# Kernel tuning notes

Measured on AMD Instinct MI355X. Metric: run time of the kernel, lower is better.

Reference implementation:

```python
import jax, jax.numpy as jnp
import numpy as np

STRIDE = (1, 2, 2)
PADDING = ((2, 2), (3, 3), (3, 3))


def setup_inputs() -> dict:
    key = jax.random.key(0)
    kx, kw, kb = jax.random.split(key, 3)
    x = jax.random.normal(kx, (8, 3, 16, 112, 112), dtype=jnp.float32)
    weight = jax.random.normal(kw, (64, 3, 5, 7, 7), dtype=jnp.float32)
    bias = jax.random.normal(kb, (64,), dtype=jnp.float32)
    return {"x": x, "weight": weight, "bias": bias}


def reference(x, weight, bias):
    # NCDHW input, OIDHW weight -> NCDHW output; same math as the
    # torch module's explicit slice-multiply-sum conv3d.
    out = jax.lax.conv_general_dilated(
        x, weight,
        window_strides=STRIDE,
        padding=PADDING,
        dimension_numbers=("NCDHW", "OIDHW", "NCDHW"),
    )
    out = out + bias[None, :, None, None, None]
    return out
```

## Files before the change

### kernel.cpp

```cpp
#include <hip/hip_runtime.h>


typedef __attribute__((ext_vector_type(8)))  short short8;
typedef __attribute__((ext_vector_type(4)))  float f32x4;
typedef __attribute__((ext_vector_type(16))) float f32x16;

#define CI 3
#define DI 16
#define HI 112
#define WI 112
#define CO 64
#define DO_ 16
#define HO 56
#define WO 56
#define HW_IN 12544
#define DHWO 50176

#define NROW 105
#define NCH 27

#define XP_ROW 120
#define XP_H   119
#define XP_D   20
#define XPAD_BYTES  (8*3*XP_D*XP_H*XP_ROW*2)
#define WBUF_OFF    XPAD_BYTES
#define WS_NEED     (WBUF_OFF + NCH*4*64*16 + 4096)

#define LR 13
#define SEG_SH (LR*XP_ROW)
#define SEG_DW (SEG_SH/2)
#define ROW_DW (XP_ROW/2)
#define ALDS_SH (18*SEG_SH + 128)

__device__ __forceinline__ unsigned short f2bf(float f) {
    unsigned u = __float_as_uint(f);
    return (unsigned short)((u + 0x7FFFu + ((u >> 16) & 1u)) >> 16);
}
__device__ __forceinline__ unsigned pk_bf16(float a, float b) {
    unsigned r;
    asm("v_cvt_pk_bf16_f32 %0, %1, %2" : "=v"(r) : "v"(a), "v"(b));
    return r;
}

__device__ __forceinline__ constexpr int rb2(int r) {
    const int rc = (r > 104) ? 104 : r;
    const int c  = rc / 35;
    const int kd = (rc / 7) % 5;
    const int kh = rc % 7;
    return (c * 6 + kd) * SEG_DW + kh * ROW_DW;
}

#define XP_THREADS (8*3*XP_D*XP_H*15)
#define XP_BLOCKS  3347

__global__ void prep_all(const float* __restrict__ x, const float* __restrict__ wgt,
                         unsigned* __restrict__ xp, short8* __restrict__ wbuf) {
    if (blockIdx.x < XP_BLOCKS) {
        const int g = blockIdx.x * 256 + threadIdx.x;
        if (g >= XP_THREADS) return;
        const int s8 = g % 15;
        int r = g / 15;
        const int hp = r % XP_H; r /= XP_H;
        const int dp = r % XP_D; r /= XP_D;
        const int c  = r % 3;
        const int n  = r / 3;
        const int din = dp - 2, hin = hp - 3;
        const bool rowok = ((unsigned)din < (unsigned)DI) && ((unsigned)hin < (unsigned)HI);
        float v[8];
        const int w0 = 8 * s8 - 3;
        if (rowok && s8 >= 1 && s8 <= 13) {
            const float* xr = x + ((n * CI + c) * DI + din) * HW_IN + hin * WI + w0;
            #pragma unroll
            for (int j = 0; j < 8; ++j) v[j] = xr[j];
        } else if (rowok && (s8 == 0 || s8 == 14)) {
            const float* xr = x + ((n * CI + c) * DI + din) * HW_IN + hin * WI;
            #pragma unroll
            for (int j = 0; j < 8; ++j) {
                const int w = w0 + j;
                v[j] = ((unsigned)w < (unsigned)WI) ? xr[w] : 0.0f;
            }
        } else {
            #pragma unroll
            for (int j = 0; j < 8; ++j) v[j] = 0.0f;
        }
        uint4 o;
        o.x = pk_bf16(v[0], v[1]); o.y = pk_bf16(v[2], v[3]);
        o.z = pk_bf16(v[4], v[5]); o.w = pk_bf16(v[6], v[7]);
        *reinterpret_cast<uint4*>(xp + 4 * (size_t)g) = o;
    } else {
        const int t = (blockIdx.x - XP_BLOCKS) * 256 + threadIdx.x;
        const int lane = t & 63;
        const int cf   = t >> 6;
        const int q    = cf & 3;
        const int a    = q & 1;
        const int ks   = q >> 1;
        const int ch   = cf >> 2;
        const int l31  = lane & 31;
        const int hl   = lane >> 5;
        const int co   = a * 32 + l31;
        const int r    = ch * 4 + ks * 2 + hl;
        const int rc   = (r > 104) ? 104 : r;
        const int c    = rc / 35;
        const int kd   = (rc / 7) % 5;
        const int kh   = rc % 7;
        const float* wsrc = wgt + (((co * CI + c) * 5 + kd) * 7 + kh) * 7;
        short8 v;
        #pragma unroll
        for (int j = 0; j < 8; ++j) {
            float w = (r < NROW && j < 7) ? wsrc[j] : 0.0f;
            v[j] = (short)f2bf(w);
        }
        wbuf[(size_t)cf * 64 + lane] = v;
    }
}

#define MFMA32(A, B, C) __builtin_amdgcn_mfma_f32_32x32x16_bf16(A, B, C, 0, 0, 0)
#define GLDS(src, dst) __builtin_amdgcn_global_load_lds( \
    (const __attribute__((address_space(1))) void*)(src), \
    (__attribute__((address_space(3))) void*)(dst), 16, 0, 0)

__launch_bounds__(512, 4)
__global__ void conv3d_v19(const unsigned short* __restrict__ xpad,
                           const short8* __restrict__ wbuf,
                           const float* __restrict__ bias,
                           float* __restrict__ out) {
    __shared__ __align__(16) unsigned short xl[ALDS_SH + 4 * 2048];

    const int tid = threadIdx.x;
    int b = ((blockIdx.x & 7) * 112) + (blockIdx.x >> 3);
    const int ht  = b % 14;  b /= 14;
    const int ddp = b & 7;
    const int n   = b >> 3;
    const int ho0 = ht * 4;
    const int dd0 = ddp * 2;

    const int lane = tid & 63;
    const int wid  = tid >> 6;

    {
        const size_t nb = (size_t)(n * CI) * XP_D;
        for (int s = wid; s < 18; s += 8) {
            const int c = s / 6;
            const int p = s - c * 6;
            const char* gsrc = (const char*)(xpad +
                ((nb + (size_t)c * XP_D + (dd0 + p)) * XP_H + 2 * ho0) * XP_ROW)
                + lane * 16;
            char* ldst = (char*)&xl[s * SEG_SH];
            GLDS(gsrc, ldst);
            GLDS(gsrc + 1024, ldst + 1024);
            GLDS(gsrc + 2048, ldst + 2048);
            if (lane < 3) GLDS(gsrc + 3072, ldst + 3072);
        }
    }
    if (wid == 0) {
        const char* gs = (const char*)wbuf + lane * 16;
        char* ad = (char*)&xl[ALDS_SH];
        GLDS(gs, ad); GLDS(gs + 1024, ad + 1024);
        GLDS(gs + 2048, ad + 2048); GLDS(gs + 3072, ad + 3072);
    } else if (wid == 1) {
        const char* gs = (const char*)(wbuf + 4 * 64) + lane * 16;
        char* ad = (char*)&xl[ALDS_SH] + 4096;
        GLDS(gs, ad); GLDS(gs + 1024, ad + 1024);
        GLDS(gs + 2048, ad + 2048); GLDS(gs + 3072, ad + 3072);
    }
    __syncthreads();

    const int ddl = wid & 1;
    const int hp  = wid >> 1;
    const int l31 = lane & 31;
    const int hl  = lane >> 5;
    const int tspB = ddl * SEG_DW + hp * (2 * ROW_DW) + l31;

    f32x16 acc[2][2];
    #pragma unroll
    for (int a = 0; a < 2; ++a) {
        f32x16 bv;
        #pragma unroll
        for (int g = 0; g < 16; ++g)
            bv[g] = bias[a * 32 + (g & 3) + 8 * (g >> 2) + 4 * hl];
        acc[a][0] = bv; acc[a][1] = bv;
    }

    const unsigned* xlu = reinterpret_cast<const unsigned*>(xl);
    union BxU { unsigned u[4]; short8 s; };

    #pragma unroll
    for (int ch = 0; ch < NCH; ++ch) {
        if (ch + 2 < NCH && wid == ((ch + 2) & 7)) {
            const char* gs = (const char*)(wbuf + (size_t)(ch + 2) * 4 * 64) + lane * 16;
            char* ad = (char*)&xl[ALDS_SH] + ((ch + 2) & 3) * 4096;
            GLDS(gs, ad); GLDS(gs + 1024, ad + 1024);
            GLDS(gs + 2048, ad + 2048); GLDS(gs + 3072, ad + 3072);
        }
        const int nks = (ch == NCH - 1) ? 1 : 2;
        BxU Bs[4];
        #pragma unroll
        for (int ks = 0; ks < 2; ++ks) {
            if (ks < nks) {
                const int r0 = ch * 4 + ks * 2;
                const int b0 = rb2(r0);
                const int b1 = rb2(r0 + 1);
                const int base = b0 + hl * (b1 - b0);
                const unsigned* xp = xlu + base + tspB;
                #pragma unroll
                for (int f = 0; f < 2; ++f) {
                    const unsigned* p = xp + f * 32;
                    Bs[ks * 2 + f].u[0] = p[0];
                    Bs[ks * 2 + f].u[1] = p[1];
                    Bs[ks * 2 + f].u[2] = p[2];
                    Bs[ks * 2 + f].u[3] = p[3];
                }
            }
        }
        short8 As[4];
        {
            const char* ab = (const char*)&xl[ALDS_SH] + (ch & 3) * 4096 + lane * 16;
            As[0] = *reinterpret_cast<const short8*>(ab);
            As[1] = *reinterpret_cast<const short8*>(ab + 1024);
            if (nks == 2) {
                As[2] = *reinterpret_cast<const short8*>(ab + 2048);
                As[3] = *reinterpret_cast<const short8*>(ab + 3072);
            }
        }
        __builtin_amdgcn_s_setprio(1);
        #pragma unroll
        for (int a = 0; a < 2; ++a) {
            #pragma unroll
            for (int f = 0; f < 2; ++f) {
                acc[a][f] = MFMA32(As[0 + a], Bs[0 + f].s, acc[a][f]);
                if (nks == 2)
                    acc[a][f] = MFMA32(As[2 + a], Bs[2 + f].s, acc[a][f]);
            }
        }
        __builtin_amdgcn_s_setprio(0);
        if ((ch & 1) && ch != NCH - 1) __syncthreads();
    }

    const int dd = dd0 + ddl;
    const int ho = ho0 + hp;
    const size_t obase = (size_t)n * CO * DHWO + (size_t)dd * 3136 + ho * WO;
    #pragma unroll
    for (int f = 0; f < 2; ++f) {
        const int wo = f * 32 + l31;
        if (f == 0 || l31 < 24) {
            #pragma unroll
            for (int a = 0; a < 2; ++a) {
                #pragma unroll
                for (int g = 0; g < 16; ++g) {
                    const int co = a * 32 + (g & 3) + 8 * (g >> 2) + 4 * hl;
                    out[obase + (size_t)co * DHWO + wo] = acc[a][f][g];
                }
            }
        }
    }
}

#define FB_LR 13
#define FB_LROWS 234
#define FB_LWS 144
#define FB_XLSZ (FB_LROWS*FB_LWS)
#define MFMA16(A, B, C) __builtin_amdgcn_mfma_f32_16x16x32_bf16(A, B, C, 0, 0, 0)

__global__ void prep_weights_fb(const float* __restrict__ wgt, short8* __restrict__ wbuf) {
    const int t    = blockIdx.x * 64 + threadIdx.x;
    const int lane = t & 63;
    const int cf   = t >> 6;
    const int l15  = lane & 15;
    const int kgrp = lane >> 4;
    const int co   = (cf & 3) * 16 + l15;
    const int rr   = (cf >> 2) * 4 + kgrp;
    const int rc   = (rr < NROW) ? rr : (NROW - 1);
    const int c    = rc / 35;
    const int kd   = (rc / 7) % 5;
    const int kh   = rc % 7;
    const float* wsrc = wgt + (((co * CI + c) * 5 + kd) * 7 + kh) * 7;
    short8 v;
    #pragma unroll
    for (int j = 0; j < 8; ++j) {
        float w = (rr < NROW && j < 7) ? wsrc[j] : 0.0f;
        v[j] = (short)f2bf(w);
    }
    wbuf[(size_t)cf * 64 + lane] = v;
}

__launch_bounds__(512, 2)
__global__ void conv3d_mfma4(const float* __restrict__ x,
                             const short8* __restrict__ wbuf,
                             const float* __restrict__ bias,
                             float* __restrict__ out) {
    __shared__ unsigned short xl[FB_XLSZ];
    __shared__ int rowg[FB_LROWS];
    __shared__ unsigned short tabr[108];

    const int tid = threadIdx.x;
    int b = blockIdx.x;
    const int ht  = b % 14;  b /= 14;
    const int ddp = b % 8;
    const int n   = b / 8;
    const int ho0 = ht * 4;
    const int dd0 = ddp * 2;

    if (tid < FB_LROWS) {
        const int c   = tid / (6 * FB_LR);
        const int rem = tid - c * (6 * FB_LR);
        const int p   = rem / FB_LR;
        const int rl  = rem - p * FB_LR;
        const int din = dd0 - 2 + p;
        const int hin = 2 * ho0 - 3 + rl;
        const bool ok = ((unsigned)din < (unsigned)DI) && ((unsigned)hin < (unsigned)HI);
        rowg[tid] = ok ? ((n * CI + c) * DI + din) * HW_IN + hin * WI : -1;
    }
    if (tid < 108) {
        const int rc = (tid < NROW) ? tid : (NROW - 1);
        const int c  = rc / 35;
        const int kd = (rc / 7) % 5;
        const int kh = rc % 7;
        tabr[tid] = (unsigned short)(((c * 6 + kd) * FB_LR + kh) * FB_LWS);
    }
    __syncthreads();

    const int lane = tid & 63;
    const int wid  = tid >> 6;

    for (int row = wid; row < FB_LROWS; row += 8) {
        const int base = rowg[row];
        unsigned short* dst = &xl[row * FB_LWS];
        if (lane < 57) {
            float v0 = 0.0f, v1 = 0.0f;
            const int w0 = 2 * lane - 1;
            if (base >= 0) {
                if (lane >= 1)  v0 = x[base + w0];
                if (lane <= 55) v1 = x[base + w0 + 1];
            }
            *reinterpret_cast<unsigned*>(&dst[2 * lane + 2]) = pk_bf16(v0, v1);
        } else {
            const int dw = (lane == 57) ? 0 : lane;
            *reinterpret_cast<unsigned*>(&dst[2 * dw]) = 0u;
        }
    }
    __syncthreads();

    const int ddl  = wid & 1;
    const int hoL  = wid >> 1;
    const int l15  = lane & 15;
    const int kgrp = lane >> 4;
    const int woff = ddl * (FB_LR * FB_LWS) + hoL * (2 * FB_LWS);

    f32x4 acc[4][4];
    #pragma unroll
    for (int a = 0; a < 4; ++a) {
        f32x4 bv;
        #pragma unroll
        for (int r = 0; r < 4; ++r) bv[r] = bias[a * 16 + kgrp * 4 + r];
        #pragma unroll
        for (int f = 0; f < 4; ++f) acc[a][f] = bv;
    }

    const short8* wbp = wbuf + lane;
    short8 Acur[4], Anxt[4];
    #pragma unroll
    for (int a = 0; a < 4; ++a) Acur[a] = wbp[a * 64];
    int tb = (int)tabr[kgrp] + woff;

    const unsigned* xlu = reinterpret_cast<const unsigned*>(xl);

    for (int ch = 0; ch < NCH; ++ch) {
        int tbn = 0;
        if (ch + 1 < NCH) {
            tbn = (int)tabr[(ch + 1) * 4 + kgrp] + woff;
            #pragma unroll
            for (int a = 0; a < 4; ++a) Anxt[a] = wbp[((ch + 1) * 4 + a) * 64];
        }
        const unsigned* xp = xlu + (tb >> 1) + l15;
        union { unsigned u[4]; short8 s; } bx[4];
        #pragma unroll
        for (int f = 0; f < 4; ++f) {
            const unsigned* p = xp + f * 16;
            bx[f].u[0] = p[0]; bx[f].u[1] = p[1];
            bx[f].u[2] = p[2]; bx[f].u[3] = p[3];
        }
        #pragma unroll
        for (int f = 0; f < 4; ++f) {
            acc[0][f] = MFMA16(Acur[0], bx[f].s, acc[0][f]);
            acc[1][f] = MFMA16(Acur[1], bx[f].s, acc[1][f]);
            acc[2][f] = MFMA16(Acur[2], bx[f].s, acc[2][f]);
            acc[3][f] = MFMA16(Acur[3], bx[f].s, acc[3][f]);
        }
        tb = tbn;
        #pragma unroll
        for (int a = 0; a < 4; ++a) Acur[a] = Anxt[a];
    }

    const int dd = dd0 + ddl;
    const int ho = ho0 + hoL;
    #pragma unroll
    for (int f = 0; f < 4; ++f) {
        const int wo = f * 16 + l15;
        if (f < 3 || l15 < 8) {
            float* op = out + (((size_t)(n * CO) * DO_ + dd) * HO + ho) * WO + wo;
            #pragma unroll
            for (int a = 0; a < 4; ++a) {
                const int co = a * 16 + kgrp * 4;
                #pragma unroll
                for (int r = 0; r < 4; ++r)
                    op[(size_t)(co + r) * DHWO] = acc[a][f][r];
            }
        }
    }
}

extern "C" void kernel_launch(void* const* d_in, const int* in_sizes, int n_in,
                              void* d_out, int out_size, void* d_ws, size_t ws_size,
                              hipStream_t stream) {
    const float* x    = (const float*)d_in[0];
    const float* wgt  = (const float*)d_in[1];
    const float* bias = (const float*)d_in[2];
    float* out        = (float*)d_out;

    if (ws_size >= (size_t)WS_NEED) {
        unsigned* xpad = (unsigned*)d_ws;
        short8* wbuf   = (short8*)((char*)d_ws + WBUF_OFF);
        hipLaunchKernelGGL(prep_all, dim3(XP_BLOCKS + 27, 1, 1), dim3(256, 1, 1), 0,
                           stream, x, wgt, xpad, wbuf);
        hipLaunchKernelGGL(conv3d_v19, dim3(896, 1, 1), dim3(512, 1, 1), 0, stream,
                           (const unsigned short*)xpad, wbuf, bias, out);
    } else {
        short8* wbuf = (short8*)d_ws;
        hipLaunchKernelGGL(prep_weights_fb, dim3(NCH * 4, 1, 1), dim3(64, 1, 1), 0,
                           stream, wgt, wbuf);
        hipLaunchKernelGGL(conv3d_mfma4, dim3(896, 1, 1), dim3(512, 1, 1), 0, stream,
                           x, wbuf, bias, out);
    }
}
```

Measured before the change: 64.10 us.

## Halve block to 4 waves, each computing 4 output columns per lane with register reuse

The conv block shrinks from 8 to 4 waves. Each wave now covers two output rows, with every lane owning four adjacent output columns. The input row is read once as two 16-byte LDS loads per k-step, and the four overlapping B fragments are built from registers by sliding, which cuts LDS reads per MFMA. Accumulators double to 8 f32x16 per lane, raising register pressure, and the smaller block with launch bounds (256,2) changes occupancy. Output stores become strided by four columns per lane, which may reduce write coalescing.

```diff
diff --git a/kernel.cpp b/kernel.cpp
--- a/kernel.cpp
+++ b/kernel.cpp
@@ -119,8 +119,8 @@
     (const __attribute__((address_space(1))) void*)(src), \
     (__attribute__((address_space(3))) void*)(dst), 16, 0, 0)
 
-__launch_bounds__(512, 4)
-__global__ void conv3d_v19(const unsigned short* __restrict__ xpad,
+__launch_bounds__(256, 2)
+__global__ void conv3d_v20(const unsigned short* __restrict__ xpad,
                            const short8* __restrict__ wbuf,
                            const float* __restrict__ bias,
                            float* __restrict__ out) {
@@ -139,7 +139,7 @@
 
     {
         const size_t nb = (size_t)(n * CI) * XP_D;
-        for (int s = wid; s < 18; s += 8) {
+        for (int s = wid; s < 18; s += 4) {
             const int c = s / 6;
             const int p = s - c * 6;
             const char* gsrc = (const char*)(xpad +
@@ -165,20 +165,24 @@
     }
     __syncthreads();
 
-    const int ddl = wid & 1;
-    const int hp  = wid >> 1;
-    const int l31 = lane & 31;
-    const int hl  = lane >> 5;
-    const int tspB = ddl * SEG_DW + hp * (2 * ROW_DW) + l31;
-
-    f32x16 acc[2][2];
+    const int ddl   = wid & 1;
+    const int hp2   = wid >> 1;
+    const int l31   = lane & 31;
+    const int hl    = lane >> 5;
+    const int l15   = l31 & 15;
+    const int hosub = l31 >> 4;
+    const int hoL   = hp2 * 2 + hosub;
+    const int tspB  = ddl * SEG_DW + hoL * (2 * ROW_DW) + 4 * l15;
+
+    f32x16 acc[2][4];
     #pragma unroll
     for (int a = 0; a < 2; ++a) {
         f32x16 bv;
         #pragma unroll
         for (int g = 0; g < 16; ++g)
             bv[g] = bias[a * 32 + (g & 3) + 8 * (g >> 2) + 4 * hl];
-        acc[a][0] = bv; acc[a][1] = bv;
+        #pragma unroll
+        for (int f = 0; f < 4; ++f) acc[a][f] = bv;
     }
 
     const unsigned* xlu = reinterpret_cast<const unsigned*>(xl);
@@ -186,31 +190,31 @@
 
     #pragma unroll
     for (int ch = 0; ch < NCH; ++ch) {
-        if (ch + 2 < NCH && wid == ((ch + 2) & 7)) {
+        if (ch + 2 < NCH && wid == ((ch + 2) & 3)) {
             const char* gs = (const char*)(wbuf + (size_t)(ch + 2) * 4 * 64) + lane * 16;
             char* ad = (char*)&xl[ALDS_SH] + ((ch + 2) & 3) * 4096;
             GLDS(gs, ad); GLDS(gs + 1024, ad + 1024);
             GLDS(gs + 2048, ad + 2048); GLDS(gs + 3072, ad + 3072);
         }
         const int nks = (ch == NCH - 1) ? 1 : 2;
-        BxU Bs[4];
-        #pragma unroll
-        for (int ks = 0; ks < 2; ++ks) {
-            if (ks < nks) {
-                const int r0 = ch * 4 + ks * 2;
-                const int b0 = rb2(r0);
-                const int b1 = rb2(r0 + 1);
-                const int base = b0 + hl * (b1 - b0);
-                const unsigned* xp = xlu + base + tspB;
-                #pragma unroll
-                for (int f = 0; f < 2; ++f) {
-                    const unsigned* p = xp + f * 32;
-                    Bs[ks * 2 + f].u[0] = p[0];
-                    Bs[ks * 2 + f].u[1] = p[1];
-                    Bs[ks * 2 + f].u[2] = p[2];
-                    Bs[ks * 2 + f].u[3] = p[3];
-                }
-            }
+        unsigned p0[8], p1[8];
+        {
+            const int r0 = ch * 4;
+            const int base = rb2(r0) + hl * (rb2(r0 + 1) - rb2(r0));
+            const unsigned* xp = xlu + base + tspB;
+            uint4 va = *reinterpret_cast<const uint4*>(xp);
+            uint4 vb = *reinterpret_cast<const uint4*>(xp + 4);
+            p0[0] = va.x; p0[1] = va.y; p0[2] = va.z; p0[3] = va.w;
+            p0[4] = vb.x; p0[5] = vb.y; p0[6] = vb.z; p0[7] = vb.w;
+        }
+        if (nks == 2) {
+            const int r0 = ch * 4 + 2;
+            const int base = rb2(r0) + hl * (rb2(r0 + 1) - rb2(r0));
+            const unsigned* xp = xlu + base + tspB;
+            uint4 va = *reinterpret_cast<const uint4*>(xp);
+            uint4 vb = *reinterpret_cast<const uint4*>(xp + 4);
+            p1[0] = va.x; p1[1] = va.y; p1[2] = va.z; p1[3] = va.w;
+            p1[4] = vb.x; p1[5] = vb.y; p1[6] = vb.z; p1[7] = vb.w;
         }
         short8 As[4];
         {
@@ -224,12 +228,21 @@
         }
         __builtin_amdgcn_s_setprio(1);
         #pragma unroll
-        for (int a = 0; a < 2; ++a) {
-            #pragma unroll
-            for (int f = 0; f < 2; ++f) {
-                acc[a][f] = MFMA32(As[0 + a], Bs[0 + f].s, acc[a][f]);
-                if (nks == 2)
-                    acc[a][f] = MFMA32(As[2 + a], Bs[2 + f].s, acc[a][f]);
+        for (int f = 0; f < 4; ++f) {
+            BxU bx;
+            bx.u[0] = p0[f]; bx.u[1] = p0[f + 1];
+            bx.u[2] = p0[f + 2]; bx.u[3] = p0[f + 3];
+            acc[0][f] = MFMA32(As[0], bx.s, acc[0][f]);
+            acc[1][f] = MFMA32(As[1], bx.s, acc[1][f]);
+        }
+        if (nks == 2) {
+            #pragma unroll
+            for (int f = 0; f < 4; ++f) {
+                BxU bx;
+                bx.u[0] = p1[f]; bx.u[1] = p1[f + 1];
+                bx.u[2] = p1[f + 2]; bx.u[3] = p1[f + 3];
+                acc[0][f] = MFMA32(As[2], bx.s, acc[0][f]);
+                acc[1][f] = MFMA32(As[3], bx.s, acc[1][f]);
             }
         }
         __builtin_amdgcn_s_setprio(0);
@@ -237,12 +250,12 @@
     }
 
     const int dd = dd0 + ddl;
-    const int ho = ho0 + hp;
+    const int ho = ho0 + hoL;
     const size_t obase = (size_t)n * CO * DHWO + (size_t)dd * 3136 + ho * WO;
-    #pragma unroll
-    for (int f = 0; f < 2; ++f) {
-        const int wo = f * 32 + l31;
-        if (f == 0 || l31 < 24) {
+    if (l15 < 14) {
+        #pragma unroll
+        for (int f = 0; f < 4; ++f) {
+            const int wo = 4 * l15 + f;
             #pragma unroll
             for (int a = 0; a < 2; ++a) {
                 #pragma unroll
@@ -422,7 +435,7 @@
         short8* wbuf   = (short8*)((char*)d_ws + WBUF_OFF);
         hipLaunchKernelGGL(prep_all, dim3(XP_BLOCKS + 27, 1, 1), dim3(256, 1, 1), 0,
                            stream, x, wgt, xpad, wbuf);
-        hipLaunchKernelGGL(conv3d_v19, dim3(896, 1, 1), dim3(512, 1, 1), 0, stream,
+        hipLaunchKernelGGL(conv3d_v20, dim3(896, 1, 1), dim3(256, 1, 1), 0, stream,
                            (const unsigned short*)xpad, wbuf, bias, out);
     } else {
         short8* wbuf = (short8*)d_ws;
```

New measurement: 78.14 us. 1.22x slower.
